# Kernel tuning notes

Hardware: AMD Instinct MI355X
Metric: run time of the kernel (lower is better)

Reference implementation:

```python
import jax, jax.numpy as jnp
import numpy as np

QLEN, MLEN = 1024, 1024
KLEN = QLEN + MLEN
BSZ = 2
D_MODEL = 1024
N_HEAD, D_HEAD = 16, 64


def setup_inputs() -> dict:
    key = jax.random.key(0)
    ks = jax.random.split(key, 8)
    s = 0.02
    return {
        "w": jax.random.normal(ks[0], (KLEN, BSZ, D_MODEL), jnp.float32),
        "r": jax.random.normal(ks[1], (KLEN, D_MODEL), jnp.float32),
        "r_w_bias": jax.random.normal(ks[2], (N_HEAD, D_HEAD), jnp.float32) * s,
        "r_r_bias": jax.random.normal(ks[3], (N_HEAD, D_HEAD), jnp.float32) * s,
        "Wq": jax.random.normal(ks[4], (D_MODEL, N_HEAD * D_HEAD), jnp.float32) * s,
        "Wkv": jax.random.normal(ks[5], (D_MODEL, 2 * N_HEAD * D_HEAD), jnp.float32) * s,
        "Wr": jax.random.normal(ks[6], (D_MODEL, N_HEAD * D_HEAD), jnp.float32) * s,
        "Wo": jax.random.normal(ks[7], (N_HEAD * D_HEAD, D_MODEL), jnp.float32) * s,
        "qlen": QLEN,
    }


def _rel_shift(x):
    # x: [qlen, klen, bsz, n_head]. Pad one zero column at the front of the
    # key axis, reinterpret flat layout as [klen+1, qlen, ...], drop row 0.
    q, k, b, n = x.shape
    x_pad = jnp.pad(x, ((0, 0), (1, 0), (0, 0), (0, 0)))
    return x_pad.reshape(k + 1, q, b, n)[1:].reshape(q, k, b, n)


def reference(w, r, r_w_bias, r_r_bias, Wq, Wkv, Wr, Wo, qlen):
    klen, bsz, _ = w.shape
    rlen = r.shape[0]
    scale = 1.0 / (D_HEAD ** 0.5)

    w_head_q = (w[-qlen:] @ Wq).reshape(qlen, bsz, N_HEAD, D_HEAD)
    kv = w @ Wkv
    w_head_k = kv[..., : N_HEAD * D_HEAD].reshape(klen, bsz, N_HEAD, D_HEAD)
    w_head_v = kv[..., N_HEAD * D_HEAD :].reshape(klen, bsz, N_HEAD, D_HEAD)
    r_head_k = (r @ Wr).reshape(rlen, N_HEAD, D_HEAD)

    AC = jnp.einsum("ibnd,jbnd->ijbn", w_head_q + r_w_bias, w_head_k)
    BD = jnp.einsum("ibnd,jnd->ijbn", w_head_q + r_r_bias, r_head_k)
    attn_score = (AC + _rel_shift(BD)) * scale

    attn_prob = jax.nn.softmax(attn_score, axis=1)
    attn_vec = jnp.einsum("ijbn,jbnd->ibnd", attn_prob, w_head_v)
    attn_vec = attn_vec.reshape(qlen, bsz, N_HEAD * D_HEAD)
    return attn_vec @ Wo
```

## Files before the change

### kernel.cpp

```cpp
#include <hip/hip_runtime.h>
#include <hip/hip_bf16.h>


#define QLENC 1024
#define KLENC 2048
#define BSZC 2
#define DMODELC 1024
#define NHC 16
#define DHC 64

typedef _Float16 half_t;
typedef __attribute__((ext_vector_type(8))) _Float16 f16x8;
typedef __attribute__((ext_vector_type(4))) float f32x4;

__device__ __forceinline__ void async_copy16(const half_t* g, half_t* l) {
    __builtin_amdgcn_global_load_lds(
        (const __attribute__((address_space(1))) void*)g,
        (__attribute__((address_space(3))) void*)l,
        16, 0, 0);
}

__global__ __launch_bounds__(256) void prep(
    const float* __restrict__ w, const float* __restrict__ r,
    const float* __restrict__ Wq, const float* __restrict__ Wkv,
    const float* __restrict__ Wr, const float* __restrict__ Wo,
    half_t* __restrict__ wh, half_t* __restrict__ rh,
    half_t* __restrict__ WqT, half_t* __restrict__ WkvT,
    half_t* __restrict__ WrT, half_t* __restrict__ WoT) {
    __shared__ __attribute__((aligned(16))) half_t T[64][72];
    int bx = blockIdx.x, t = threadIdx.x;
    if (bx < 3072) {
        const float* s; half_t* d; size_t base;
        if (bx < 2048) { s = w; d = wh; base = (size_t)bx * 2048; }
        else           { s = r; d = rh; base = (size_t)(bx - 2048) * 2048; }
        size_t i = base + (size_t)t * 8;
        const float4* sp = (const float4*)(s + i);
        float4 f0 = sp[0], f1 = sp[1];
        half_t h[8];
        h[0] = (half_t)f0.x; h[1] = (half_t)f0.y; h[2] = (half_t)f0.z; h[3] = (half_t)f0.w;
        h[4] = (half_t)f1.x; h[5] = (half_t)f1.y; h[6] = (half_t)f1.z; h[7] = (half_t)f1.w;
        *(uint4*)(d + i) = *(uint4*)&h[0];
        return;
    }
    int b2 = bx - 3072;
    const float* W; half_t* Wt; int N, tx, ty;
    if (b2 < 256)       { W = Wq;  Wt = WqT;  N = 1024; tx = b2 & 15;         ty = b2 >> 4; }
    else if (b2 < 768)  { int c = b2 - 256;  W = Wkv; Wt = WkvT; N = 2048; tx = c & 31; ty = c >> 5; }
    else if (b2 < 1024) { int c = b2 - 768;  W = Wr;  Wt = WrT;  N = 1024; tx = c & 15; ty = c >> 4; }
    else                { int c = b2 - 1024; W = Wo;  Wt = WoT;  N = 1024; tx = c & 15; ty = c >> 4; }
    const int K = 1024;
    int n0 = tx * 64, k0 = ty * 64;
    int r_ = t >> 2, c_ = (t & 3) << 4;
    const float4* s = (const float4*)&W[(size_t)(k0 + r_) * N + n0 + c_];
    float4 f0 = s[0], f1 = s[1], f2 = s[2], f3 = s[3];
    half_t h[16];
    h[0] = (half_t)f0.x; h[1] = (half_t)f0.y; h[2] = (half_t)f0.z; h[3] = (half_t)f0.w;
    h[4] = (half_t)f1.x; h[5] = (half_t)f1.y; h[6] = (half_t)f1.z; h[7] = (half_t)f1.w;
    h[8] = (half_t)f2.x; h[9] = (half_t)f2.y; h[10] = (half_t)f2.z; h[11] = (half_t)f2.w;
    h[12] = (half_t)f3.x; h[13] = (half_t)f3.y; h[14] = (half_t)f3.z; h[15] = (half_t)f3.w;
    *(uint4*)&T[r_][c_] = *(uint4*)&h[0];
    *(uint4*)&T[r_][c_ + 8] = *(uint4*)&h[8];
    __syncthreads();
    half_t vals[16];
#pragma unroll
    for (int u = 0; u < 16; u++) vals[u] = T[c_ + u][r_];
    *(uint4*)&Wt[(size_t)(n0 + r_) * K + k0 + c_] = *(uint4*)&vals[0];
    *(uint4*)&Wt[(size_t)(n0 + r_) * K + k0 + c_ + 8] = *(uint4*)&vals[8];
}

__global__ __launch_bounds__(256) void proj_fused(
    const half_t* __restrict__ wh, const half_t* __restrict__ rh,
    const half_t* __restrict__ WqT, const half_t* __restrict__ WkvT,
    const half_t* __restrict__ WrT,
    half_t* __restrict__ qw, half_t* __restrict__ qr,
    half_t* __restrict__ kh, half_t* __restrict__ vt,
    half_t* __restrict__ rk,
    const float* __restrict__ rwb, const float* __restrict__ rrb) {
    __shared__ __attribute__((aligned(16))) half_t SM[128 * 136];
    half_t (*As)[64] = (half_t(*)[64])SM;
    half_t (*Bs)[64] = (half_t(*)[64])(SM + 128 * 64);
    half_t (*LT)[136] = (half_t(*)[136])SM;

    int bid = blockIdx.x;
    int mode, tx, ty;
    const half_t* A; const half_t* Bt;
    if (bid < 512)      { mode = 1; tx = bid & 15, ty = bid >> 4; A = wh; Bt = WkvT; }
    else if (bid < 640) { int c = bid - 512; mode = 0; tx = c & 7; ty = c >> 3;
                          A = wh + (size_t)QLENC * BSZC * DMODELC; Bt = WqT; }
    else                { int c = bid - 640; mode = 2; tx = c & 7; ty = c >> 3;
                          A = rh; Bt = WrT; }

    int t = threadIdx.x;
    int w = t >> 6, ln = t & 63, quad = ln >> 4, l15 = ln & 15;
    int m0 = ty * 128, n0 = tx * 128;
    int rbase = 64 * (w >> 1), cbase = 64 * (w & 1);
    int lrow = ln >> 3, lcol = (ln & 7) * 8;

    f32x4 acc[4][4];
#pragma unroll
    for (int i = 0; i < 4; i++)
#pragma unroll
        for (int j = 0; j < 4; j++) acc[i][j] = (f32x4){0.f, 0.f, 0.f, 0.f};

    for (int k0 = 0; k0 < 1024; k0 += 64) {
        __syncthreads();
#pragma unroll
        for (int j = 0; j < 4; j++) {
            int r8 = w * 32 + j * 8;
            async_copy16(&A[(size_t)(m0 + r8 + lrow) * 1024 + k0 + lcol], &As[r8][0]);
            async_copy16(&Bt[(size_t)(n0 + r8 + lrow) * 1024 + k0 + lcol], &Bs[r8][0]);
        }
        __syncthreads();
#pragma unroll
        for (int kk = 0; kk < 2; kk++) {
            f16x8 af[4], bfr[4];
#pragma unroll
            for (int rb = 0; rb < 4; rb++)
                af[rb] = *(const f16x8*)&As[rbase + rb * 16 + l15][kk * 32 + quad * 8];
#pragma unroll
            for (int cb = 0; cb < 4; cb++)
                bfr[cb] = *(const f16x8*)&Bs[cbase + cb * 16 + l15][kk * 32 + quad * 8];
#pragma unroll
            for (int rb = 0; rb < 4; rb++)
#pragma unroll
                for (int cb = 0; cb < 4; cb++)
                    acc[rb][cb] = __builtin_amdgcn_mfma_f32_16x16x32_f16(
                        af[rb], bfr[cb], acc[rb][cb], 0, 0, 0);
        }
    }

    if (mode == 1 && tx >= 8) {
        __syncthreads();
#pragma unroll
        for (int rb = 0; rb < 4; rb++)
#pragma unroll
            for (int cb = 0; cb < 4; cb++)
#pragma unroll
                for (int reg = 0; reg < 4; reg++) {
                    int lr_ = rbase + 16 * rb + quad * 4 + reg;
                    int lc_ = cbase + 16 * cb + l15;
                    LT[lc_][lr_] = (half_t)acc[rb][cb][reg];
                }
        __syncthreads();
#pragma unroll
        for (int pass = 0; pass < 8; pass++) {
            int g = pass * 32 + (t >> 3), s_ = t & 7;
            int lc_ = g >> 1, b_ = g & 1;
            half_t tmp[8];
#pragma unroll
            for (int k = 0; k < 8; k++) tmp[k] = LT[lc_][b_ + 2 * (s_ * 8 + k)];
            int gc = n0 - 1024 + lc_;
            int hh = gc >> 6, d_ = gc & 63;
            int p0 = (m0 >> 1) + s_ * 8;
            *(uint4*)&vt[(((size_t)(b_ * NHC + hh)) * DHC + d_) * KLENC + p0] = *(uint4*)&tmp[0];
        }
        return;
    }

#pragma unroll
    for (int rb = 0; rb < 4; rb++)
#pragma unroll
        for (int cb = 0; cb < 4; cb++)
#pragma unroll
            for (int reg = 0; reg < 4; reg++) {
                int gr = m0 + rbase + 16 * rb + quad * 4 + reg;
                int gc = n0 + cbase + 16 * cb + l15;
                float v = acc[rb][cb][reg];
                if (mode == 1) {
                    int p_ = gr >> 1, b_ = gr & 1;
                    int n_ = gc >> 6, d_ = gc & 63;
                    kh[(((size_t)(b_ * NHC + n_)) * KLENC + p_) * DHC + d_] = (half_t)v;
                } else if (mode == 0) {
                    int p_ = gr >> 1, b_ = gr & 1, n_ = gc >> 6, d_ = gc & 63;
                    size_t idx = (((size_t)(b_ * NHC + n_)) * QLENC + p_) * DHC + d_;
                    qw[idx] = (half_t)(v + rwb[gc]);
                    qr[idx] = (half_t)(v + rrb[gc]);
                } else {
                    int n_ = gc >> 6, d_ = gc & 63;
                    rk[(((size_t)n_) * KLENC + gr) * DHC + d_] = (half_t)v;
                }
            }
}

__global__ __launch_bounds__(256) void gemm_out(
    const half_t* __restrict__ A, const half_t* __restrict__ Bt,
    float* __restrict__ o) {
    __shared__ __attribute__((aligned(16))) half_t As[128][64];
    __shared__ __attribute__((aligned(16))) half_t Bs[128][64];

    int t = threadIdx.x;
    int w = t >> 6, ln = t & 63, quad = ln >> 4, l15 = ln & 15;
    int m0 = blockIdx.y * 128, n0 = blockIdx.x * 128;
    int rbase = 64 * (w >> 1), cbase = 64 * (w & 1);
    int lrow = ln >> 3, lcol = (ln & 7) * 8;

    f32x4 acc[4][4];
#pragma unroll
    for (int i = 0; i < 4; i++)
#pragma unroll
        for (int j = 0; j < 4; j++) acc[i][j] = (f32x4){0.f, 0.f, 0.f, 0.f};

    for (int k0 = 0; k0 < 1024; k0 += 64) {
        __syncthreads();
#pragma unroll
        for (int j = 0; j < 4; j++) {
            int r8 = w * 32 + j * 8;
            async_copy16(&A[(size_t)(m0 + r8 + lrow) * 1024 + k0 + lcol], &As[r8][0]);
            async_copy16(&Bt[(size_t)(n0 + r8 + lrow) * 1024 + k0 + lcol], &Bs[r8][0]);
        }
        __syncthreads();
#pragma unroll
        for (int kk = 0; kk < 2; kk++) {
            f16x8 af[4], bfr[4];
#pragma unroll
            for (int rb = 0; rb < 4; rb++)
                af[rb] = *(const f16x8*)&As[rbase + rb * 16 + l15][kk * 32 + quad * 8];
#pragma unroll
            for (int cb = 0; cb < 4; cb++)
                bfr[cb] = *(const f16x8*)&Bs[cbase + cb * 16 + l15][kk * 32 + quad * 8];
#pragma unroll
            for (int rb = 0; rb < 4; rb++)
#pragma unroll
                for (int cb = 0; cb < 4; cb++)
                    acc[rb][cb] = __builtin_amdgcn_mfma_f32_16x16x32_f16(
                        af[rb], bfr[cb], acc[rb][cb], 0, 0, 0);
        }
    }

#pragma unroll
    for (int rb = 0; rb < 4; rb++)
#pragma unroll
        for (int cb = 0; cb < 4; cb++)
#pragma unroll
            for (int reg = 0; reg < 4; reg++) {
                int gr = m0 + rbase + 16 * rb + quad * 4 + reg;
                int gc = n0 + cbase + 16 * cb + l15;
                o[(size_t)gr * 1024 + gc] = acc[rb][cb][reg];
            }
}

__global__ __launch_bounds__(256, 3) void attn_fused(
    const half_t* __restrict__ qw, const half_t* __restrict__ qr,
    const half_t* __restrict__ kh, const half_t* __restrict__ vt,
    const half_t* __restrict__ rk, float* __restrict__ po,
    float* __restrict__ pl) {
    __shared__ __attribute__((aligned(16))) half_t Ks[64][72];
    __shared__ __attribute__((aligned(16))) half_t Vs[64][72];
    __shared__ __attribute__((aligned(16))) half_t RKs[128][72];
    __shared__ __attribute__((aligned(16))) half_t TP[4][16][88];

    int n = blockIdx.x, i0 = blockIdx.y * 64;
    int z = blockIdx.z, b = z >> 1, s = z & 1;
    int jt0 = s * 16, jt1 = jt0 + 16;
    int t = threadIdx.x, w = t >> 6, ln = t & 63, quad = ln >> 4, l15 = ln & 15;
    int lr = t >> 2, lc = (t & 3) << 4;
    int q4 = quad * 4;
    int wq = w * 16 + q4;
    size_t bn = (size_t)(b * NHC + n);
    const half_t* rkn = rk + (size_t)n * KLENC * DHC;
    half_t (*TPw)[88] = TP[w];

    f16x8 aqw[2], aq1[2], aq2[2];
    {
        int row1 = i0 + w * 16 + l15;
        int row2 = row1 + 1; if (row2 > QLENC - 1) row2 = QLENC - 1;
#pragma unroll
        for (int kk = 0; kk < 2; kk++) {
            aqw[kk] = *(const f16x8*)&qw[((bn * QLENC) + row1) * DHC + kk * 32 + quad * 8];
            aq1[kk] = *(const f16x8*)&qr[((bn * QLENC) + row1) * DHC + kk * 32 + quad * 8];
            aq2[kk] = *(const f16x8*)&qr[((bn * QLENC) + row2) * DHC + kk * 32 + quad * 8];
        }
    }

    int rrl = t >> 1, rh = (t & 1) * 32;

    uint4 pk0, pk1, pv0, pv1, pr0, pr1, pr2, pr3;
    {
        int j0 = jt0 * 64;
        int D = j0 - i0;
        int mb = (D <= 1024) ? (960 + D) : (D - 1089);
        int rrow = mb + rrl; rrow = rrow < 0 ? 0 : (rrow > KLENC - 1 ? KLENC - 1 : rrow);
        const uint4* ks = (const uint4*)&kh[((bn * KLENC) + j0 + lr) * DHC + lc];
        const uint4* vs = (const uint4*)&vt[((bn * DHC) + lr) * KLENC + j0 + lc];
        pk0 = ks[0]; pk1 = ks[1]; pv0 = vs[0]; pv1 = vs[1];
        const uint4* rs = (const uint4*)&rkn[(size_t)rrow * DHC + rh];
        pr0 = rs[0]; pr1 = rs[1]; pr2 = rs[2]; pr3 = rs[3];
    }

    f32x4 O[4];
#pragma unroll
    for (int i = 0; i < 4; i++) O[i] = (f32x4){0.f, 0.f, 0.f, 0.f};
    float lsum[4] = {0.f, 0.f, 0.f, 0.f};
    const float scale = 0.125f;

    for (int jt = jt0; jt < jt1; jt++) {
        int j0 = jt * 64;
        int D = j0 - i0;
        bool need1 = (D <= 1024), need2 = (D >= 1024);

        __syncthreads();
        *(uint4*)&Ks[lr][lc] = pk0; *(uint4*)&Ks[lr][lc + 8] = pk1;
        *(uint4*)&Vs[lr][lc] = pv0; *(uint4*)&Vs[lr][lc + 8] = pv1;
        *(uint4*)&RKs[rrl][rh] = pr0;      *(uint4*)&RKs[rrl][rh + 8] = pr1;
        *(uint4*)&RKs[rrl][rh + 16] = pr2; *(uint4*)&RKs[rrl][rh + 24] = pr3;
        __syncthreads();

        if (jt + 1 < jt1) {
            int j0n = j0 + 64, Dn = j0n - i0;
            int mbn = (Dn <= 1024) ? (960 + Dn) : (Dn - 1089);
            int rrown = mbn + rrl; rrown = rrown < 0 ? 0 : (rrown > KLENC - 1 ? KLENC - 1 : rrown);
            const uint4* ks = (const uint4*)&kh[((bn * KLENC) + j0n + lr) * DHC + lc];
            const uint4* vs = (const uint4*)&vt[((bn * DHC) + lr) * KLENC + j0n + lc];
            pk0 = ks[0]; pk1 = ks[1]; pv0 = vs[0]; pv1 = vs[1];
            const uint4* rs = (const uint4*)&rkn[(size_t)rrown * DHC + rh];
            pr0 = rs[0]; pr1 = rs[1]; pr2 = rs[2]; pr3 = rs[3];
        }

        f32x4 sa[4];
#pragma unroll
        for (int cb = 0; cb < 4; cb++) sa[cb] = (f32x4){0.f, 0.f, 0.f, 0.f};
#pragma unroll
        for (int kk = 0; kk < 2; kk++) {
#pragma unroll
            for (int cb = 0; cb < 4; cb++) {
                f16x8 bk = *(const f16x8*)&Ks[cb * 16 + l15][kk * 32 + quad * 8];
                sa[cb] = __builtin_amdgcn_mfma_f32_16x16x32_f16(aqw[kk], bk, sa[cb], 0, 0, 0);
            }
        }

        float bdv[4][4];
#pragma unroll
        for (int cb = 0; cb < 4; cb++)
#pragma unroll
            for (int reg = 0; reg < 4; reg++) bdv[cb][reg] = 0.f;

        if (need1) {
            f32x4 tacc[5];
#pragma unroll
            for (int c = 0; c < 5; c++) tacc[c] = (f32x4){0.f, 0.f, 0.f, 0.f};
#pragma unroll
            for (int kk = 0; kk < 2; kk++) {
#pragma unroll
                for (int c = 0; c < 5; c++) {
                    f16x8 bk = *(const f16x8*)&RKs[(3 - w + c) * 16 + l15][kk * 32 + quad * 8];
                    tacc[c] = __builtin_amdgcn_mfma_f32_16x16x32_f16(aq1[kk], bk, tacc[c], 0, 0, 0);
                }
            }
#pragma unroll
            for (int c = 0; c < 5; c++)
#pragma unroll
                for (int reg = 0; reg < 4; reg++)
                    TPw[q4 + reg][c * 16 + l15] = (half_t)tacc[c][reg];
#pragma unroll
            for (int reg = 0; reg < 4; reg++) {
                int icl = q4 + reg, ic = w * 16 + icl;
#pragma unroll
                for (int cb = 0; cb < 4; cb++) {
                    int jc = cb * 16 + l15;
                    int delta = D + jc - ic;
                    if (delta <= 1024) bdv[cb][reg] = (float)TPw[icl][15 + jc - icl];
                }
            }
        }
        if (need2) {
            if (need1) {
                int mb2 = D - 1089;
                int rrow2 = mb2 + rrl; rrow2 = rrow2 < 0 ? 0 : (rrow2 > KLENC - 1 ? KLENC - 1 : rrow2);
                const uint4* rs2 = (const uint4*)&rkn[(size_t)rrow2 * DHC + rh];
                uint4 t0 = rs2[0], t1 = rs2[1], t2 = rs2[2], t3 = rs2[3];
                __syncthreads();
                *(uint4*)&RKs[rrl][rh] = t0;      *(uint4*)&RKs[rrl][rh + 8] = t1;
                *(uint4*)&RKs[rrl][rh + 16] = t2; *(uint4*)&RKs[rrl][rh + 24] = t3;
                __syncthreads();
            }
            f32x4 tacc[5];
#pragma unroll
            for (int c = 0; c < 5; c++) tacc[c] = (f32x4){0.f, 0.f, 0.f, 0.f};
#pragma unroll
            for (int kk = 0; kk < 2; kk++) {
#pragma unroll
                for (int c = 0; c < 5; c++) {
                    f16x8 bk = *(const f16x8*)&RKs[(3 - w + c) * 16 + l15][kk * 32 + quad * 8];
                    tacc[c] = __builtin_amdgcn_mfma_f32_16x16x32_f16(aq2[kk], bk, tacc[c], 0, 0, 0);
                }
            }
#pragma unroll
            for (int c = 0; c < 5; c++)
#pragma unroll
                for (int reg = 0; reg < 4; reg++)
                    TPw[q4 + reg][c * 16 + l15] = (half_t)tacc[c][reg];
#pragma unroll
            for (int reg = 0; reg < 4; reg++) {
                int icl = q4 + reg, ic = w * 16 + icl;
#pragma unroll
                for (int cb = 0; cb < 4; cb++) {
                    int jc = cb * 16 + l15;
                    int delta = D + jc - ic;
                    if (delta >= 1026) bdv[cb][reg] = (float)TPw[icl][15 + jc - icl];
                }
            }
        }

        float p[4][4];
#pragma unroll
        for (int reg = 0; reg < 4; reg++) {
            float ps = 0.f;
#pragma unroll
            for (int cb = 0; cb < 4; cb++) {
                float e = __expf((sa[cb][reg] + bdv[cb][reg]) * scale);
                e = fminf(e, 60000.f);
                p[cb][reg] = e; ps += e;
            }
            lsum[reg] += ps;
        }

#pragma unroll
        for (int cb = 0; cb < 4; cb++)
#pragma unroll
            for (int reg = 0; reg < 4; reg++)
                TPw[q4 + reg][cb * 16 + l15] = (half_t)p[cb][reg];
#pragma unroll
        for (int kk = 0; kk < 2; kk++) {
            f16x8 pa = *(const f16x8*)&TPw[l15][kk * 32 + quad * 8];
#pragma unroll
            for (int db = 0; db < 4; db++) {
                f16x8 vb = *(const f16x8*)&Vs[db * 16 + l15][kk * 32 + quad * 8];
                O[db] = __builtin_amdgcn_mfma_f32_16x16x32_f16(pa, vb, O[db], 0, 0, 0);
            }
        }
    }

    size_t pobase = ((size_t)s * 32 + bn) * QLENC;
#pragma unroll
    for (int db = 0; db < 4; db++)
#pragma unroll
        for (int reg = 0; reg < 4; reg++)
            po[(pobase + i0 + wq + reg) * 64 + db * 16 + l15] = O[db][reg];
#pragma unroll
    for (int reg = 0; reg < 4; reg++) {
        float tot = lsum[reg];
#pragma unroll
        for (int off = 1; off < 16; off <<= 1) tot += __shfl_xor(tot, off, 64);
        if (l15 == 0) pl[pobase + i0 + wq + reg] = tot;
    }
}

__global__ __launch_bounds__(256) void combine(
    const float* __restrict__ po, const float* __restrict__ pl,
    half_t* __restrict__ av) {
    int gid = blockIdx.x * 256 + threadIdx.x;
    int d0 = (gid & 7) * 8;
    int i = (gid >> 3) & 1023;
    int bn = gid >> 13;
    size_t rowoff = (size_t)bn * QLENC + i;
    size_t base = rowoff * 64 + d0;
    const size_t S = (size_t)32 * QLENC * 64;
    float4 a0 = *(const float4*)&po[base];
    float4 a1 = *(const float4*)&po[base + 4];
    float4 b0 = *(const float4*)&po[S + base];
    float4 b1 = *(const float4*)&po[S + base + 4];
    float invl = 1.0f / (pl[rowoff] + pl[(size_t)32 * QLENC + rowoff]);
    half_t h[8];
    h[0] = (half_t)((a0.x + b0.x) * invl); h[1] = (half_t)((a0.y + b0.y) * invl);
    h[2] = (half_t)((a0.z + b0.z) * invl); h[3] = (half_t)((a0.w + b0.w) * invl);
    h[4] = (half_t)((a1.x + b1.x) * invl); h[5] = (half_t)((a1.y + b1.y) * invl);
    h[6] = (half_t)((a1.z + b1.z) * invl); h[7] = (half_t)((a1.w + b1.w) * invl);
    int b = bn >> 4, n = bn & 15;
    *(uint4*)&av[((size_t)i * BSZC + b) * DMODELC + n * 64 + d0] = *(uint4*)&h[0];
}

extern "C" void kernel_launch(void* const* d_in, const int* in_sizes, int n_in,
                              void* d_out, int out_size, void* d_ws, size_t ws_size,
                              hipStream_t stream) {
    const float* w   = (const float*)d_in[0];
    const float* r   = (const float*)d_in[1];
    const float* rwb = (const float*)d_in[2];
    const float* rrb = (const float*)d_in[3];
    const float* Wq  = (const float*)d_in[4];
    const float* Wkv = (const float*)d_in[5];
    const float* Wr  = (const float*)d_in[6];
    const float* Wo  = (const float*)d_in[7];
    float* out = (float*)d_out;

    half_t* ws = (half_t*)d_ws;
    half_t* qw   = ws; ws += (size_t)BSZC * NHC * QLENC * DHC;
    half_t* qr   = ws; ws += (size_t)BSZC * NHC * QLENC * DHC;
    half_t* kh   = ws; ws += (size_t)BSZC * NHC * KLENC * DHC;
    half_t* vt   = ws; ws += (size_t)BSZC * NHC * KLENC * DHC;
    half_t* rk   = ws; ws += (size_t)NHC * KLENC * DHC;
    half_t* av   = ws; ws += (size_t)QLENC * BSZC * DMODELC;
    half_t* WoT  = ws; ws += (size_t)DMODELC * DMODELC;
    half_t* WqT  = ws; ws += (size_t)DMODELC * DMODELC;
    half_t* WkvT = ws; ws += (size_t)2 * DMODELC * DMODELC;
    half_t* WrT  = ws; ws += (size_t)DMODELC * DMODELC;
    half_t* wh   = ws; ws += (size_t)KLENC * BSZC * DMODELC;
    half_t* rh   = ws; ws += (size_t)KLENC * DMODELC;

    float* po = (float*)WqT;
    float* pl = po + (size_t)2 * 32 * QLENC * 64;

    dim3 blk(256);
    prep<<<dim3(4352), blk, 0, stream>>>(w, r, Wq, Wkv, Wr, Wo,
                                         wh, rh, WqT, WkvT, WrT, WoT);
    proj_fused<<<dim3(768), blk, 0, stream>>>(
        wh, rh, WqT, WkvT, WrT, qw, qr, kh, vt, rk, rwb, rrb);
    attn_fused<<<dim3(NHC, QLENC / 64, BSZC * 2), blk, 0, stream>>>(
        qw, qr, kh, vt, rk, po, pl);
    combine<<<dim3(1024), blk, 0, stream>>>(po, pl, av);
    gemm_out<<<dim3(8, 16), blk, 0, stream>>>(av, WoT, out);

    (void)in_sizes; (void)n_in; (void)out_size; (void)ws_size;
}
```

Measured before the change: 268.9 us.

## Enlarge attention query tile to 128 rows so each wave computes two row tiles

The fused attention kernel now handles 128 query rows per block, with each wave owning two 16-row tiles. Each K/V/RK tile loaded into shared memory is therefore reused across twice as many queries, and the grid shrinks by half. The relative-position band grows to 192 rows. In the mixed case the second RK band is now prefetched into registers before the score MFMAs instead of being loaded in a blocking way. The cost is more registers and shared memory, so launch bounds drop from 3 to 2 blocks per CU, and there are fewer blocks to spread across the CUs.

```diff
diff --git a/kernel.cpp b/kernel.cpp
--- a/kernel.cpp
+++ b/kernel.cpp
@@ -239,209 +239,234 @@
             }
 }
 
-__global__ __launch_bounds__(256, 3) void attn_fused(
+__global__ __launch_bounds__(256, 2) void attn_fused(
     const half_t* __restrict__ qw, const half_t* __restrict__ qr,
     const half_t* __restrict__ kh, const half_t* __restrict__ vt,
     const half_t* __restrict__ rk, float* __restrict__ po,
     float* __restrict__ pl) {
     __shared__ __attribute__((aligned(16))) half_t Ks[64][72];
     __shared__ __attribute__((aligned(16))) half_t Vs[64][72];
-    __shared__ __attribute__((aligned(16))) half_t RKs[128][72];
-    __shared__ __attribute__((aligned(16))) half_t TP[4][16][88];
-
-    int n = blockIdx.x, i0 = blockIdx.y * 64;
+    __shared__ __attribute__((aligned(16))) half_t RKs[192][72];
+    __shared__ __attribute__((aligned(16))) half_t TP[4][32][104];
+
+    int n = blockIdx.x, i0 = blockIdx.y * 128;
     int z = blockIdx.z, b = z >> 1, s = z & 1;
     int jt0 = s * 16, jt1 = jt0 + 16;
     int t = threadIdx.x, w = t >> 6, ln = t & 63, quad = ln >> 4, l15 = ln & 15;
     int lr = t >> 2, lc = (t & 3) << 4;
     int q4 = quad * 4;
-    int wq = w * 16 + q4;
+    int rkb = 96 - 32 * w;
     size_t bn = (size_t)(b * NHC + n);
     const half_t* rkn = rk + (size_t)n * KLENC * DHC;
-    half_t (*TPw)[88] = TP[w];
-
-    f16x8 aqw[2], aq1[2], aq2[2];
+    half_t (*TPw)[104] = TP[w];
+
+    f16x8 aqw[2][2], aq1[2][2], aq2[2][2];
+#pragma unroll
+    for (int rt = 0; rt < 2; rt++) {
+        int r1 = i0 + w * 32 + rt * 16 + l15;
+        int r2 = r1 + 1; if (r2 > QLENC - 1) r2 = QLENC - 1;
+#pragma unroll
+        for (int kk = 0; kk < 2; kk++) {
+            aqw[rt][kk] = *(const f16x8*)&qw[((bn * QLENC) + r1) * DHC + kk * 32 + quad * 8];
+            aq1[rt][kk] = *(const f16x8*)&qr[((bn * QLENC) + r1) * DHC + kk * 32 + quad * 8];
+            aq2[rt][kk] = *(const f16x8*)&qr[((bn * QLENC) + r2) * DHC + kk * 32 + quad * 8];
+        }
+    }
+
+    uint4 pk0, pk1, pv0, pv1, pr[6];
     {
-        int row1 = i0 + w * 16 + l15;
-        int row2 = row1 + 1; if (row2 > QLENC - 1) row2 = QLENC - 1;
-#pragma unroll
-        for (int kk = 0; kk < 2; kk++) {
-            aqw[kk] = *(const f16x8*)&qw[((bn * QLENC) + row1) * DHC + kk * 32 + quad * 8];
-            aq1[kk] = *(const f16x8*)&qr[((bn * QLENC) + row1) * DHC + kk * 32 + quad * 8];
-            aq2[kk] = *(const f16x8*)&qr[((bn * QLENC) + row2) * DHC + kk * 32 + quad * 8];
-        }
-    }
-
-    int rrl = t >> 1, rh = (t & 1) * 32;
-
-    uint4 pk0, pk1, pv0, pv1, pr0, pr1, pr2, pr3;
-    {
-        int j0 = jt0 * 64;
-        int D = j0 - i0;
-        int mb = (D <= 1024) ? (960 + D) : (D - 1089);
-        int rrow = mb + rrl; rrow = rrow < 0 ? 0 : (rrow > KLENC - 1 ? KLENC - 1 : rrow);
+        int j0 = jt0 * 64, D = j0 - i0;
         const uint4* ks = (const uint4*)&kh[((bn * KLENC) + j0 + lr) * DHC + lc];
         const uint4* vs = (const uint4*)&vt[((bn * DHC) + lr) * KLENC + j0 + lc];
         pk0 = ks[0]; pk1 = ks[1]; pv0 = vs[0]; pv1 = vs[1];
-        const uint4* rs = (const uint4*)&rkn[(size_t)rrow * DHC + rh];
-        pr0 = rs[0]; pr1 = rs[1]; pr2 = rs[2]; pr3 = rs[3];
-    }
-
-    f32x4 O[4];
-#pragma unroll
-    for (int i = 0; i < 4; i++) O[i] = (f32x4){0.f, 0.f, 0.f, 0.f};
-    float lsum[4] = {0.f, 0.f, 0.f, 0.f};
+        int mb = (D <= 1088) ? (896 + D) : (D - 1153);
+#pragma unroll
+        for (int i = 0; i < 6; i++) {
+            int rr = mb + i * 32 + (t >> 3);
+            rr = rr < 0 ? 0 : (rr > KLENC - 1 ? KLENC - 1 : rr);
+            pr[i] = *(const uint4*)&rkn[(size_t)rr * DHC + (t & 7) * 8];
+        }
+    }
+
+    f32x4 O[2][4];
+#pragma unroll
+    for (int rt = 0; rt < 2; rt++)
+#pragma unroll
+        for (int i = 0; i < 4; i++) O[rt][i] = (f32x4){0.f, 0.f, 0.f, 0.f};
+    float lsum[2][4] = {{0.f, 0.f, 0.f, 0.f}, {0.f, 0.f, 0.f, 0.f}};
     const float scale = 0.125f;
 
     for (int jt = jt0; jt < jt1; jt++) {
         int j0 = jt * 64;
         int D = j0 - i0;
-        bool need1 = (D <= 1024), need2 = (D >= 1024);
+        bool need1 = (D <= 1088), need2 = (D >= 1024);
+        bool mixed = need1 && need2;
 
         __syncthreads();
         *(uint4*)&Ks[lr][lc] = pk0; *(uint4*)&Ks[lr][lc + 8] = pk1;
         *(uint4*)&Vs[lr][lc] = pv0; *(uint4*)&Vs[lr][lc + 8] = pv1;
-        *(uint4*)&RKs[rrl][rh] = pr0;      *(uint4*)&RKs[rrl][rh + 8] = pr1;
-        *(uint4*)&RKs[rrl][rh + 16] = pr2; *(uint4*)&RKs[rrl][rh + 24] = pr3;
+#pragma unroll
+        for (int i = 0; i < 6; i++)
+            *(uint4*)&RKs[i * 32 + (t >> 3)][(t & 7) * 8] = pr[i];
         __syncthreads();
 
         if (jt + 1 < jt1) {
             int j0n = j0 + 64, Dn = j0n - i0;
-            int mbn = (Dn <= 1024) ? (960 + Dn) : (Dn - 1089);
-            int rrown = mbn + rrl; rrown = rrown < 0 ? 0 : (rrown > KLENC - 1 ? KLENC - 1 : rrown);
             const uint4* ks = (const uint4*)&kh[((bn * KLENC) + j0n + lr) * DHC + lc];
             const uint4* vs = (const uint4*)&vt[((bn * DHC) + lr) * KLENC + j0n + lc];
             pk0 = ks[0]; pk1 = ks[1]; pv0 = vs[0]; pv1 = vs[1];
-            const uint4* rs = (const uint4*)&rkn[(size_t)rrown * DHC + rh];
-            pr0 = rs[0]; pr1 = rs[1]; pr2 = rs[2]; pr3 = rs[3];
-        }
-
-        f32x4 sa[4];
-#pragma unroll
-        for (int cb = 0; cb < 4; cb++) sa[cb] = (f32x4){0.f, 0.f, 0.f, 0.f};
-#pragma unroll
-        for (int kk = 0; kk < 2; kk++) {
+            int mbn = (Dn <= 1088) ? (896 + Dn) : (Dn - 1153);
+#pragma unroll
+            for (int i = 0; i < 6; i++) {
+                int rr = mbn + i * 32 + (t >> 3);
+                rr = rr < 0 ? 0 : (rr > KLENC - 1 ? KLENC - 1 : rr);
+                pr[i] = *(const uint4*)&rkn[(size_t)rr * DHC + (t & 7) * 8];
+            }
+        }
+        uint4 qb[6];
+        if (mixed) {
+            int mbB = D - 1153;
+#pragma unroll
+            for (int i = 0; i < 6; i++) {
+                int rr = mbB + i * 32 + (t >> 3);
+                rr = rr < 0 ? 0 : (rr > KLENC - 1 ? KLENC - 1 : rr);
+                qb[i] = *(const uint4*)&rkn[(size_t)rr * DHC + (t & 7) * 8];
+            }
+        }
+
+        f32x4 sa[2][4];
+#pragma unroll
+        for (int rt = 0; rt < 2; rt++)
+#pragma unroll
+            for (int cb = 0; cb < 4; cb++) sa[rt][cb] = (f32x4){0.f, 0.f, 0.f, 0.f};
+#pragma unroll
+        for (int kk = 0; kk < 2; kk++)
 #pragma unroll
             for (int cb = 0; cb < 4; cb++) {
                 f16x8 bk = *(const f16x8*)&Ks[cb * 16 + l15][kk * 32 + quad * 8];
-                sa[cb] = __builtin_amdgcn_mfma_f32_16x16x32_f16(aqw[kk], bk, sa[cb], 0, 0, 0);
-            }
-        }
-
-        float bdv[4][4];
-#pragma unroll
-        for (int cb = 0; cb < 4; cb++)
-#pragma unroll
-            for (int reg = 0; reg < 4; reg++) bdv[cb][reg] = 0.f;
-
-        if (need1) {
-            f32x4 tacc[5];
-#pragma unroll
-            for (int c = 0; c < 5; c++) tacc[c] = (f32x4){0.f, 0.f, 0.f, 0.f};
+                sa[0][cb] = __builtin_amdgcn_mfma_f32_16x16x32_f16(aqw[0][kk], bk, sa[0][cb], 0, 0, 0);
+                sa[1][cb] = __builtin_amdgcn_mfma_f32_16x16x32_f16(aqw[1][kk], bk, sa[1][cb], 0, 0, 0);
+            }
+
+        float bdv[2][4][4];
+#pragma unroll
+        for (int rt = 0; rt < 2; rt++)
+#pragma unroll
+            for (int cb = 0; cb < 4; cb++)
+#pragma unroll
+                for (int reg = 0; reg < 4; reg++) bdv[rt][cb][reg] = 0.f;
+
+#pragma unroll
+        for (int rt = 0; rt < 2; rt++) {
+            f32x4 tacc[6];
+#pragma unroll
+            for (int c = 0; c < 6; c++) tacc[c] = (f32x4){0.f, 0.f, 0.f, 0.f};
 #pragma unroll
             for (int kk = 0; kk < 2; kk++) {
-#pragma unroll
-                for (int c = 0; c < 5; c++) {
-                    f16x8 bk = *(const f16x8*)&RKs[(3 - w + c) * 16 + l15][kk * 32 + quad * 8];
-                    tacc[c] = __builtin_amdgcn_mfma_f32_16x16x32_f16(aq1[kk], bk, tacc[c], 0, 0, 0);
+                f16x8 aqA = need1 ? aq1[rt][kk] : aq2[rt][kk];
+#pragma unroll
+                for (int c = 0; c < 6; c++) {
+                    f16x8 bk = *(const f16x8*)&RKs[rkb + c * 16 + l15][kk * 32 + quad * 8];
+                    tacc[c] = __builtin_amdgcn_mfma_f32_16x16x32_f16(aqA, bk, tacc[c], 0, 0, 0);
                 }
             }
 #pragma unroll
-            for (int c = 0; c < 5; c++)
+            for (int c = 0; c < 6; c++)
 #pragma unroll
                 for (int reg = 0; reg < 4; reg++)
-                    TPw[q4 + reg][c * 16 + l15] = (half_t)tacc[c][reg];
+                    TPw[rt * 16 + q4 + reg][c * 16 + l15] = (half_t)tacc[c][reg];
 #pragma unroll
             for (int reg = 0; reg < 4; reg++) {
-                int icl = q4 + reg, ic = w * 16 + icl;
+                int icl = rt * 16 + q4 + reg, ic = w * 32 + icl;
 #pragma unroll
                 for (int cb = 0; cb < 4; cb++) {
                     int jc = cb * 16 + l15;
                     int delta = D + jc - ic;
-                    if (delta <= 1024) bdv[cb][reg] = (float)TPw[icl][15 + jc - icl];
+                    bool take = need1 ? (delta <= 1024) : (delta >= 1026);
+                    if (take) bdv[rt][cb][reg] = (float)TPw[icl][31 + jc - icl];
                 }
             }
         }
-        if (need2) {
-            if (need1) {
-                int mb2 = D - 1089;
-                int rrow2 = mb2 + rrl; rrow2 = rrow2 < 0 ? 0 : (rrow2 > KLENC - 1 ? KLENC - 1 : rrow2);
-                const uint4* rs2 = (const uint4*)&rkn[(size_t)rrow2 * DHC + rh];
-                uint4 t0 = rs2[0], t1 = rs2[1], t2 = rs2[2], t3 = rs2[3];
-                __syncthreads();
-                *(uint4*)&RKs[rrl][rh] = t0;      *(uint4*)&RKs[rrl][rh + 8] = t1;
-                *(uint4*)&RKs[rrl][rh + 16] = t2; *(uint4*)&RKs[rrl][rh + 24] = t3;
-                __syncthreads();
-            }
-            f32x4 tacc[5];
-#pragma unroll
-            for (int c = 0; c < 5; c++) tacc[c] = (f32x4){0.f, 0.f, 0.f, 0.f};
-#pragma unroll
-            for (int kk = 0; kk < 2; kk++) {
-#pragma unroll
-                for (int c = 0; c < 5; c++) {
-                    f16x8 bk = *(const f16x8*)&RKs[(3 - w + c) * 16 + l15][kk * 32 + quad * 8];
-                    tacc[c] = __builtin_amdgcn_mfma_f32_16x16x32_f16(aq2[kk], bk, tacc[c], 0, 0, 0);
+        if (mixed) {
+            __syncthreads();
+#pragma unroll
+            for (int i = 0; i < 6; i++)
+                *(uint4*)&RKs[i * 32 + (t >> 3)][(t & 7) * 8] = qb[i];
+            __syncthreads();
+#pragma unroll
+            for (int rt = 0; rt < 2; rt++) {
+                f32x4 tacc[6];
+#pragma unroll
+                for (int c = 0; c < 6; c++) tacc[c] = (f32x4){0.f, 0.f, 0.f, 0.f};
+#pragma unroll
+                for (int kk = 0; kk < 2; kk++)
+#pragma unroll
+                    for (int c = 0; c < 6; c++) {
+                        f16x8 bk = *(const f16x8*)&RKs[rkb + c * 16 + l15][kk * 32 + quad * 8];
+                        tacc[c] = __builtin_amdgcn_mfma_f32_16x16x32_f16(aq2[rt][kk], bk, tacc[c], 0, 0, 0);
+                    }
+#pragma unroll
+                for (int c = 0; c < 6; c++)
+#pragma unroll
+                    for (int reg = 0; reg < 4; reg++)
+                        TPw[rt * 16 + q4 + reg][c * 16 + l15] = (half_t)tacc[c][reg];
+#pragma unroll
+                for (int reg = 0; reg < 4; reg++) {
+                    int icl = rt * 16 + q4 + reg, ic = w * 32 + icl;
+#pragma unroll
+                    for (int cb = 0; cb < 4; cb++) {
+                        int jc = cb * 16 + l15;
+                        int delta = D + jc - ic;
+                        if (delta >= 1026) bdv[rt][cb][reg] = (float)TPw[icl][31 + jc - icl];
+                    }
                 }
             }
-#pragma unroll
-            for (int c = 0; c < 5; c++)
-#pragma unroll
-                for (int reg = 0; reg < 4; reg++)
-                    TPw[q4 + reg][c * 16 + l15] = (half_t)tacc[c][reg];
+        }
+
+#pragma unroll
+        for (int rt = 0; rt < 2; rt++)
 #pragma unroll
             for (int reg = 0; reg < 4; reg++) {
-                int icl = q4 + reg, ic = w * 16 + icl;
+                float ps = 0.f;
 #pragma unroll
                 for (int cb = 0; cb < 4; cb++) {
-                    int jc = cb * 16 + l15;
-                    int delta = D + jc - ic;
-                    if (delta >= 1026) bdv[cb][reg] = (float)TPw[icl][15 + jc - icl];
+                    float e = __expf((sa[rt][cb][reg] + bdv[rt][cb][reg]) * scale);
+                    e = fminf(e, 60000.f);
+                    TPw[rt * 16 + q4 + reg][cb * 16 + l15] = (half_t)e;
+                    ps += e;
                 }
-            }
-        }
-
-        float p[4][4];
-#pragma unroll
-        for (int reg = 0; reg < 4; reg++) {
-            float ps = 0.f;
-#pragma unroll
-            for (int cb = 0; cb < 4; cb++) {
-                float e = __expf((sa[cb][reg] + bdv[cb][reg]) * scale);
-                e = fminf(e, 60000.f);
-                p[cb][reg] = e; ps += e;
-            }
-            lsum[reg] += ps;
-        }
-
-#pragma unroll
-        for (int cb = 0; cb < 4; cb++)
-#pragma unroll
-            for (int reg = 0; reg < 4; reg++)
-                TPw[q4 + reg][cb * 16 + l15] = (half_t)p[cb][reg];
+                lsum[rt][reg] += ps;
+            }
+
 #pragma unroll
         for (int kk = 0; kk < 2; kk++) {
-            f16x8 pa = *(const f16x8*)&TPw[l15][kk * 32 + quad * 8];
+            f16x8 pa0 = *(const f16x8*)&TPw[l15][kk * 32 + quad * 8];
+            f16x8 pa1 = *(const f16x8*)&TPw[16 + l15][kk * 32 + quad * 8];
 #pragma unroll
             for (int db = 0; db < 4; db++) {
                 f16x8 vb = *(const f16x8*)&Vs[db * 16 + l15][kk * 32 + quad * 8];
-                O[db] = __builtin_amdgcn_mfma_f32_16x16x32_f16(pa, vb, O[db], 0, 0, 0);
+                O[0][db] = __builtin_amdgcn_mfma_f32_16x16x32_f16(pa0, vb, O[0][db], 0, 0, 0);
+                O[1][db] = __builtin_amdgcn_mfma_f32_16x16x32_f16(pa1, vb, O[1][db], 0, 0, 0);
             }
         }
     }
 
     size_t pobase = ((size_t)s * 32 + bn) * QLENC;
 #pragma unroll
-    for (int db = 0; db < 4; db++)
-#pragma unroll
-        for (int reg = 0; reg < 4; reg++)
-            po[(pobase + i0 + wq + reg) * 64 + db * 16 + l15] = O[db][reg];
-#pragma unroll
-    for (int reg = 0; reg < 4; reg++) {
-        float tot = lsum[reg];
-#pragma unroll
-        for (int off = 1; off < 16; off <<= 1) tot += __shfl_xor(tot, off, 64);
-        if (l15 == 0) pl[pobase + i0 + wq + reg] = tot;
+    for (int rt = 0; rt < 2; rt++) {
+        int rowb = i0 + w * 32 + rt * 16 + q4;
+#pragma unroll
+        for (int db = 0; db < 4; db++)
+#pragma unroll
+            for (int reg = 0; reg < 4; reg++)
+                po[(pobase + rowb + reg) * 64 + db * 16 + l15] = O[rt][db][reg];
+#pragma unroll
+        for (int reg = 0; reg < 4; reg++) {
+            float tot = lsum[rt][reg];
+#pragma unroll
+            for (int off = 1; off < 16; off <<= 1) tot += __shfl_xor(tot, off, 64);
+            if (l15 == 0) pl[pobase + rowb + reg] = tot;
+        }
     }
 }
 
@@ -504,7 +529,7 @@
                                          wh, rh, WqT, WkvT, WrT, WoT);
     proj_fused<<<dim3(768), blk, 0, stream>>>(
         wh, rh, WqT, WkvT, WrT, qw, qr, kh, vt, rk, rwb, rrb);
-    attn_fused<<<dim3(NHC, QLENC / 64, BSZC * 2), blk, 0, stream>>>(
+    attn_fused<<<dim3(NHC, QLENC / 128, BSZC * 2), blk, 0, stream>>>(
         qw, qr, kh, vt, rk, po, pl);
     combine<<<dim3(1024), blk, 0, stream>>>(po, pl, av);
     gemm_out<<<dim3(8, 16), blk, 0, stream>>>(av, WoT, out);
```

New measurement: 365.9 us. 1.36x slower.
